# Performance work log

Hardware: AMD Instinct MI355X
Metric: run time of the kernel (lower is better)

The kernel has to match this reference:

```python
import jax, jax.numpy as jnp
import numpy as np

N_HEAD = 16
LN_EPS = 1e-5


def _ln(x, w, b):
    # torch LayerNorm computed in float32 then cast back (see LayerNorm.forward)
    xf = x.astype(jnp.float32)
    mu = jnp.mean(xf, axis=-1, keepdims=True)
    var = jnp.mean(jnp.square(xf - mu), axis=-1, keepdims=True)
    return ((xf - mu) * jax.lax.rsqrt(var + LN_EPS) * w + b).astype(x.dtype)


def setup_inputs() -> dict:
    key = jax.random.key(0)
    ks = jax.random.split(key, 16)
    B, S, C = 4, 1500, 1024
    A = 256  # adapter_dim
    F = 4 * C
    s = 0.02
    return {
        "x": jax.random.normal(ks[0], (B, S, C), jnp.float32),
        "Wq": jax.random.normal(ks[1], (C, C), jnp.float32) * s,
        "bq": jnp.zeros((C,), jnp.float32),
        "Wk": jax.random.normal(ks[2], (C, C), jnp.float32) * s,
        "Wv": jax.random.normal(ks[3], (C, C), jnp.float32) * s,
        "bv": jnp.zeros((C,), jnp.float32),
        "Wo": jax.random.normal(ks[4], (C, C), jnp.float32) * s,
        "bo": jnp.zeros((C,), jnp.float32),
        "ln_attn_w": jnp.ones((C,), jnp.float32),
        "ln_attn_b": jnp.zeros((C,), jnp.float32),
        "W1": jax.random.normal(ks[5], (F, C), jnp.float32) * s,
        "b1": jnp.zeros((F,), jnp.float32),
        "W2": jax.random.normal(ks[6], (C, F), jnp.float32) * s,
        "b2": jnp.zeros((C,), jnp.float32),
        "ln_mlp_w": jnp.ones((C,), jnp.float32),
        "ln_mlp_b": jnp.zeros((C,), jnp.float32),
        "Wds": jax.random.normal(ks[7], (A, C), jnp.float32) * s,
        "bds": jnp.zeros((A,), jnp.float32),
        "Wus": jax.random.normal(ks[8], (C, A), jnp.float32) * s,
        "bus": jnp.zeros((C,), jnp.float32),
    }


def reference(x, Wq, bq, Wk, Wv, bv, Wo, bo, ln_attn_w, ln_attn_b,
              W1, b1, W2, b2, ln_mlp_w, ln_mlp_b, Wds, bds, Wus, bus):
    B, S, C = x.shape
    H = N_HEAD
    D = C // H
    scale = D ** -0.25  # applied to both q and k, per qkv_attention

    # --- self-attention ---
    h = _ln(x, ln_attn_w, ln_attn_b)
    q = (h @ Wq.T + bq).reshape(B, S, H, D) * scale
    k = (h @ Wk.T).reshape(B, S, H, D) * scale  # key has no bias
    v = (h @ Wv.T + bv).reshape(B, S, H, D)
    qk = jnp.einsum("bqhd,bkhd->bhqk", q, k).astype(jnp.float32)
    w = jax.nn.softmax(qk, axis=-1).astype(x.dtype)
    wv = jnp.einsum("bhqk,bkhd->bqhd", w, v).reshape(B, S, C)
    x = x + (wv @ Wo.T + bo)

    # --- MLP (exact GELU, as nn.GELU default) ---
    h = _ln(x, ln_mlp_w, ln_mlp_b)
    x = x + (jax.nn.gelu(h @ W1.T + b1, approximate=False) @ W2.T + b2)

    # --- bottleneck adapter: x + us(gelu(ds(x))) ---
    x = x + (jax.nn.gelu(x @ Wds.T + bds, approximate=False) @ Wus.T + bus)
    return x
```

## Files before the change

kernel.cpp:

```cpp
#include <hip/hip_runtime.h>
#include <hip/hip_bf16.h>
#include <math.h>

typedef __bf16 bf16;
typedef __bf16 bf16x8 __attribute__((ext_vector_type(8)));
typedef float  f32x4  __attribute__((ext_vector_type(4)));

__device__ __forceinline__ bf16x8 zero8() { bf16x8 z = {}; return z; }

__device__ __forceinline__ void load16_lds(const bf16* g, bf16* l) {
    __builtin_amdgcn_global_load_lds(
        (__attribute__((address_space(1))) void*)(g),
        (__attribute__((address_space(3))) void*)(l), 16, 0, 0);
}

__device__ __forceinline__ float gelu_f(float x) {
    float u = 1.5957691216057308f * (x + 0.044715f * x * x * x);
    float e = __expf(u);
    float th = 1.0f - 2.0f / (1.0f + e);
    return 0.5f * x * (1.0f + th);
}

struct ConvArgs {
    const float* src[19];
    bf16* dst[19];
    int n[19];
    int bstart[20];
};
__global__ __launch_bounds__(256) void convert_many(ConvArgs a) {
    int blk = blockIdx.x;
    int s = 0;
    while (blk >= a.bstart[s + 1]) s++;
    const float* src = a.src[s];
    bf16* dst = a.dst[s];
    int n = a.n[s];
    int i0 = (blk - a.bstart[s]) * 2048;
#pragma unroll
    for (int e = 0; e < 8; e++) {
        int i = i0 + threadIdx.x + e * 256;
        if (i < n) dst[i] = (bf16)src[i];
    }
}

__global__ void zero_kernel(bf16* dst, int n) {
    int i = blockIdx.x * blockDim.x + threadIdx.x;
    if (i < n) dst[i] = (bf16)0.0f;
}

template<class XT>
__global__ __launch_bounds__(256) void ln_kernel(
    const XT* __restrict__ X, const bf16* __restrict__ w,
    const bf16* __restrict__ b, bf16* __restrict__ out)
{
    const int C = 1024;
    const int row = blockIdx.x;
    const int tid = threadIdx.x;
    const XT* xr = X + (size_t)row * C;
    float x0 = (float)xr[tid * 4 + 0], x1 = (float)xr[tid * 4 + 1];
    float x2 = (float)xr[tid * 4 + 2], x3 = (float)xr[tid * 4 + 3];
    float s  = x0 + x1 + x2 + x3;
    float sq = x0*x0 + x1*x1 + x2*x2 + x3*x3;
#pragma unroll
    for (int off = 32; off >= 1; off >>= 1) {
        s  += __shfl_xor(s,  off, 64);
        sq += __shfl_xor(sq, off, 64);
    }
    __shared__ float red[8];
    int wave = tid >> 6;
    if ((tid & 63) == 0) { red[wave] = s; red[4 + wave] = sq; }
    __syncthreads();
    float ts = red[0] + red[1] + red[2] + red[3];
    float tq = red[4] + red[5] + red[6] + red[7];
    float mean = ts * (1.0f / C);
    float var  = tq * (1.0f / C) - mean * mean;
    float rstd = rsqrtf(var + 1e-5f);
    float w0 = (float)w[tid*4+0], w1 = (float)w[tid*4+1], w2 = (float)w[tid*4+2], w3 = (float)w[tid*4+3];
    float b0 = (float)b[tid*4+0], b1 = (float)b[tid*4+1], b2 = (float)b[tid*4+2], b3 = (float)b[tid*4+3];
    bf16* orow = out + (size_t)row * C + tid * 4;
    orow[0] = (bf16)((x0 - mean) * rstd * w0 + b0);
    orow[1] = (bf16)((x1 - mean) * rstd * w1 + b1);
    orow[2] = (bf16)((x2 - mean) * rstd * w2 + b2);
    orow[3] = (bf16)((x3 - mean) * rstd * w3 + b3);
}

template<int ACT, int OMODE, class RT, class OT>
__global__ __launch_bounds__(256) void gemm_kernel(
    const bf16* __restrict__ A, const bf16* __restrict__ W,
    const bf16* __restrict__ bias, const RT* __restrict__ resid,
    OT* __restrict__ out, bf16* __restrict__ out_k, bf16* __restrict__ out_v,
    int M, int N, int K, float scale, int gmT, int gnT, int mQ)
{
    const int lin = blockIdx.x;
    const int xcd = lin & 7;
    const int t_  = lin >> 3;
    const int mt_ = (xcd & 3) + 4 * (t_ % mQ);
    const int nt_ = (xcd >> 2) + 2 * (t_ / mQ);
    if (mt_ >= gmT || nt_ >= gnT) return;
    const int m0 = mt_ * 128;
    const int n0 = nt_ * 128;

    __shared__ __align__(16) bf16 As[16 * 512];
    __shared__ __align__(16) bf16 Bs[16 * 512];
    const int tid = threadIdx.x;
    const int wave = tid >> 6, lane = tid & 63;
    const int lane15 = lane & 15, quad = lane >> 4;
    const int wm0 = (wave >> 1) * 64;
    const int wn0 = (wave & 1) * 64;
    f32x4 acc[4][4] = {};

    int ra0 = m0 + (2 * wave)     * 16 + lane15; if (ra0 > M - 1) ra0 = M - 1;
    int ra1 = m0 + (2 * wave + 1) * 16 + lane15; if (ra1 > M - 1) ra1 = M - 1;
    const int rb0 = n0 + (2 * wave)     * 16 + lane15;
    const int rb1 = n0 + (2 * wave + 1) * 16 + lane15;
    const bf16* a0 = A + (size_t)ra0 * K + quad * 8;
    const bf16* a1 = A + (size_t)ra1 * K + quad * 8;
    const bf16* w0 = W + (size_t)rb0 * K + quad * 8;
    const bf16* w1 = W + (size_t)rb1 * K + quad * 8;

    for (int k0 = 0; k0 < K; k0 += 64) {
#pragma unroll
        for (int kk = 0; kk < 2; kk++) {
            load16_lds(a0 + k0 + kk * 32, &As[((2 * wave)     * 2 + kk) * 512]);
            load16_lds(a1 + k0 + kk * 32, &As[((2 * wave + 1) * 2 + kk) * 512]);
            load16_lds(w0 + k0 + kk * 32, &Bs[((2 * wave)     * 2 + kk) * 512]);
            load16_lds(w1 + k0 + kk * 32, &Bs[((2 * wave + 1) * 2 + kk) * 512]);
        }
        __syncthreads();
#pragma unroll
        for (int kk = 0; kk < 2; kk++) {
            bf16x8 af[4], bfr[4];
#pragma unroll
            for (int t = 0; t < 4; t++) {
                af[t]  = *(const bf16x8*)(&As[(((wm0 >> 4) + t) * 2 + kk) * 512 + lane * 8]);
                bfr[t] = *(const bf16x8*)(&Bs[(((wn0 >> 4) + t) * 2 + kk) * 512 + lane * 8]);
            }
#pragma unroll
            for (int mt = 0; mt < 4; mt++)
#pragma unroll
                for (int nt = 0; nt < 4; nt++)
                    acc[mt][nt] = __builtin_amdgcn_mfma_f32_16x16x32_bf16(
                        af[mt], bfr[nt], acc[mt][nt], 0, 0, 0);
        }
        __syncthreads();
    }

#pragma unroll
    for (int mt = 0; mt < 4; mt++) {
#pragma unroll
        for (int r = 0; r < 4; r++) {
            int gm = m0 + wm0 + mt * 16 + quad * 4 + r;
            if (gm >= M) continue;
#pragma unroll
            for (int nt = 0; nt < 4; nt++) {
                int gn = n0 + wn0 + nt * 16 + lane15;
                float v = acc[mt][nt][r];
                if (bias) v += (float)bias[gn];
                if (OMODE == 2) {
                    if (gn < 2048) {
                        v *= scale;
                        if (gn < 1024) v *= 1.4426950408889634f;
                    }
                } else v *= scale;
                if (ACT == 1) v = gelu_f(v);
                if (OMODE == 2) {
                    if (gn < 1024) {
                        ((bf16*)out)[(size_t)gm * 1024 + gn] = (bf16)v;
                    } else if (gn < 2048) {
                        out_k[(size_t)gm * 1024 + (gn - 1024)] = (bf16)v;
                    } else {
                        int gg = gn - 2048;
                        int bb = gm / 1500;
                        int ss = gm - bb * 1500;
                        int hh = gg >> 6, dd = gg & 63;
                        out_v[(((size_t)bb * 16 + hh) * 64 + dd) * 1536 + ss] = (bf16)v;
                    }
                } else {
                    if (resid) v += (float)resid[(size_t)gm * N + gn];
                    out[(size_t)gm * N + gn] = (OT)v;
                }
            }
        }
    }
}

__global__ __launch_bounds__(256) void flash_attn_kernel(
    const bf16* __restrict__ Q, const bf16* __restrict__ Km,
    const bf16* __restrict__ Vt, bf16* __restrict__ O)
{
    const int S = 1500, C = 1024, SP = 1536;
    const int LDP = 72;
    __shared__ __align__(16) bf16 Ks[8 * 512];
    __shared__ __align__(16) bf16 Vs[8 * 512];
    __shared__ __align__(16) bf16 Ps[4 * 16 * LDP];
    const int tid = threadIdx.x;
    const int wave = tid >> 6, lane = tid & 63;
    const int lane15 = lane & 15, quad = lane >> 4;
    const int bh = blockIdx.y;
    const int q0 = blockIdx.x * 64;
    const size_t headoff = (size_t)(bh >> 4) * S * C + (size_t)(bh & 15) * 64;
    const size_t vtoff   = (size_t)bh * 64 * SP;

    bf16x8 qf[2];
    int qr = q0 + wave * 16 + lane15; if (qr > S - 1) qr = S - 1;
    qf[0] = *(const bf16x8*)(Q + headoff + (size_t)qr * C + quad * 8);
    qf[1] = *(const bf16x8*)(Q + headoff + (size_t)qr * C + 32 + quad * 8);

    const bf16* vbase = Vt + vtoff + (size_t)(wave * 16 + lane15) * SP + quad * 8;

    float m_run[4], l_part[4];
    f32x4 o_acc[4] = {};
#pragma unroll
    for (int r = 0; r < 4; r++) { m_run[r] = 4.0f; l_part[r] = 0.0f; }

    for (int kt = 0; kt < 24; kt++) {
        const int j0 = kt * 64;
        int kr = j0 + wave * 16 + lane15; if (kr > S - 1) kr = S - 1;
        const bf16* kbase = Km + headoff + (size_t)kr * C + quad * 8;
#pragma unroll
        for (int kk = 0; kk < 2; kk++) {
            load16_lds(kbase + kk * 32,      &Ks[(wave * 2 + kk) * 512]);
            load16_lds(vbase + j0 + kk * 32, &Vs[(wave * 2 + kk) * 512]);
        }
        __syncthreads();

        f32x4 s[4] = {};
#pragma unroll
        for (int kk = 0; kk < 2; kk++) {
#pragma unroll
            for (int nt = 0; nt < 4; nt++) {
                bf16x8 kf = *(const bf16x8*)(&Ks[(nt * 2 + kk) * 512 + lane * 8]);
                s[nt] = __builtin_amdgcn_mfma_f32_16x16x32_bf16(qf[kk], kf, s[nt], 0, 0, 0);
            }
        }
        if (kt == 23) {
#pragma unroll
            for (int nt = 0; nt < 4; nt++) {
                if (j0 + nt * 16 + lane15 >= S) {
#pragma unroll
                    for (int r = 0; r < 4; r++) s[nt][r] = -1e30f;
                }
            }
        }

        float tm[4];
#pragma unroll
        for (int r = 0; r < 4; r++)
            tm[r] = fmaxf(fmaxf(s[0][r], s[1][r]), fmaxf(s[2][r], s[3][r]));
        bool rec = (tm[0] > m_run[0]) | (tm[1] > m_run[1]) |
                   (tm[2] > m_run[2]) | (tm[3] > m_run[3]);
        if (__any(rec)) {
#pragma unroll
            for (int r = 0; r < 4; r++) {
                float rm = tm[r];
#pragma unroll
                for (int off = 1; off < 16; off <<= 1) rm = fmaxf(rm, __shfl_xor(rm, off, 64));
                float mnew  = fmaxf(m_run[r], rm);
                float alpha = __builtin_amdgcn_exp2f(m_run[r] - mnew);
                m_run[r] = mnew;
                l_part[r] *= alpha;
#pragma unroll
                for (int dt = 0; dt < 4; dt++) o_acc[dt][r] *= alpha;
            }
        }

#pragma unroll
        for (int nt = 0; nt < 4; nt++) {
#pragma unroll
            for (int r = 0; r < 4; r++) {
                float p = __builtin_amdgcn_exp2f(s[nt][r] - m_run[r]);
                l_part[r] += p;
                Ps[wave * 16 * LDP + (quad * 4 + r) * LDP + nt * 16 + lane15] = (bf16)p;
            }
        }
        asm volatile("s_waitcnt lgkmcnt(0)" ::: "memory");
        __builtin_amdgcn_sched_barrier(0);
#pragma unroll
        for (int kk = 0; kk < 2; kk++) {
            bf16x8 pf = *(const bf16x8*)(&Ps[wave * 16 * LDP + lane15 * LDP + kk * 32 + quad * 8]);
#pragma unroll
            for (int dt = 0; dt < 4; dt++) {
                bf16x8 vf = *(const bf16x8*)(&Vs[(dt * 2 + kk) * 512 + lane * 8]);
                o_acc[dt] = __builtin_amdgcn_mfma_f32_16x16x32_bf16(pf, vf, o_acc[dt], 0, 0, 0);
            }
        }
        __syncthreads();
    }

    float l_inv[4];
#pragma unroll
    for (int r = 0; r < 4; r++) {
        float ls = l_part[r];
#pragma unroll
        for (int off = 1; off < 16; off <<= 1) ls += __shfl_xor(ls, off, 64);
        l_inv[r] = 1.0f / ls;
    }

#pragma unroll
    for (int dt = 0; dt < 4; dt++) {
#pragma unroll
        for (int r = 0; r < 4; r++) {
            int row = q0 + wave * 16 + quad * 4 + r;
            if (row < S) {
                float v = o_acc[dt][r] * l_inv[r];
                O[headoff + (size_t)row * C + dt * 16 + lane15] = (bf16)v;
            }
        }
    }
}

extern "C" void kernel_launch(void* const* d_in, const int* in_sizes, int n_in,
                              void* d_out, int out_size, void* d_ws, size_t ws_size,
                              hipStream_t stream) {
    float* out = (float*)d_out;
    const float* x_f32 = (const float*)d_in[0];
    const int M = 6000, Cc = 1024, F = 4096, Aa = 256;
    const size_t MC = (size_t)M * Cc;
    const size_t VT_ELEMS = (size_t)64 * 64 * 1536;
    bf16* ws = (bf16*)d_ws;

    bf16* h1   = ws;
    bf16* kbuf = ws + MC;
    bf16* Vt   = ws + 2 * MC;
    bf16* g    = ws + 2 * MC + VT_ELEMS;
    bf16* q    = (bf16*)d_out;
    bf16* wv   = h1;
    bf16* x1   = q;
    bf16* h2   = kbuf;
    bf16* x2   = Vt;
    bf16* aact = kbuf;

    size_t off = 2 * MC + VT_ELEMS + (size_t)M * F;
    bf16* Wqkv = ws + off; off += (size_t)3 * 1024 * 1024;
    bf16* bqkv = ws + off; off += 3072;
    bf16* sWo  = ws + off; off += (size_t)1024 * 1024;
    bf16* sbo  = ws + off; off += 1024;
    bf16* slnw = ws + off; off += 1024;
    bf16* slnb = ws + off; off += 1024;
    bf16* sW1  = ws + off; off += (size_t)4096 * 1024;
    bf16* sb1  = ws + off; off += 4096;
    bf16* sW2  = ws + off; off += (size_t)1024 * 4096;
    bf16* sb2  = ws + off; off += 1024;
    bf16* sln2w = ws + off; off += 1024;
    bf16* sln2b = ws + off; off += 1024;
    bf16* sWds = ws + off; off += (size_t)256 * 1024;
    bf16* sbds = ws + off; off += 256;
    bf16* sWus = ws + off; off += (size_t)1024 * 256;
    bf16* sbus = ws + off; off += 1024;

    ConvArgs ca;
    const int srcidx[19] = {1, 3, 4, 2, 5, 6, 7, 8, 9, 10, 11, 12, 13, 14, 15, 16, 17, 18, 19};
    bf16* dsts[19] = {Wqkv, Wqkv + 1048576, Wqkv + 2097152, bqkv, bqkv + 2048,
                      sWo, sbo, slnw, slnb, sW1, sb1, sW2, sb2, sln2w, sln2b,
                      sWds, sbds, sWus, sbus};
    int bacc = 0;
    for (int i = 0; i < 19; i++) {
        ca.src[i] = (const float*)d_in[srcidx[i]];
        ca.dst[i] = dsts[i];
        ca.n[i] = in_sizes[srcidx[i]];
        ca.bstart[i] = bacc;
        bacc += (ca.n[i] + 2047) / 2048;
    }
    ca.bstart[19] = bacc;

    dim3 blk(256);
    convert_many<<<bacc, blk, 0, stream>>>(ca);
    zero_kernel<<<4, blk, 0, stream>>>(bqkv + 1024, 1024);

    const float scale = 0.35355339059327373f;
    const int gmT = 47, mQ = 12;
    auto grid_for = [&](int gnT) { int nQ = (gnT + 1) >> 1; return dim3(8 * mQ * nQ); };

    ln_kernel<float><<<M, blk, 0, stream>>>(x_f32, slnw, slnb, h1);
    gemm_kernel<0, 2, bf16, bf16><<<grid_for(24), blk, 0, stream>>>(
        h1, Wqkv, bqkv, (const bf16*)nullptr, q, kbuf, Vt, M, 3072, Cc, scale, gmT, 24, mQ);
    dim3 ga(24, 64);
    flash_attn_kernel<<<ga, blk, 0, stream>>>(q, kbuf, Vt, wv);
    gemm_kernel<0, 0, float, bf16><<<grid_for(8), blk, 0, stream>>>(
        wv, sWo, sbo, x_f32, x1, nullptr, nullptr, M, Cc, Cc, 1.0f, gmT, 8, mQ);
    ln_kernel<bf16><<<M, blk, 0, stream>>>(x1, sln2w, sln2b, h2);
    gemm_kernel<1, 0, bf16, bf16><<<grid_for(32), blk, 0, stream>>>(
        h2, sW1, sb1, (const bf16*)nullptr, g, nullptr, nullptr, M, F, Cc, 1.0f, gmT, 32, mQ);
    gemm_kernel<0, 0, bf16, bf16><<<grid_for(8), blk, 0, stream>>>(
        g, sW2, sb2, x1, x2, nullptr, nullptr, M, Cc, F, 1.0f, gmT, 8, mQ);
    gemm_kernel<1, 0, bf16, bf16><<<grid_for(2), blk, 0, stream>>>(
        x2, sWds, sbds, (const bf16*)nullptr, aact, nullptr, nullptr, M, Aa, Cc, 1.0f, gmT, 2, mQ);
    gemm_kernel<0, 0, bf16, float><<<grid_for(8), blk, 0, stream>>>(
        aact, sWus, sbus, x2, out, nullptr, nullptr, M, Cc, Aa, 1.0f, gmT, 8, mQ);
}
```

Measured before the change: 809.2 us.

## Double-buffer LDS tiles in GEMM and flash attention to overlap loads with MFMA

Both the GEMM and flash-attention kernels now keep two LDS buffers. The next K-tile (or K/V tile) is issued through global_load_lds before the MFMA work on the current tile, so global latency overlaps compute, and each loop step ends with a single wait plus barrier instead of two __syncthreads. This doubles LDS use per block: 64 KB for the GEMM, which may reduce occupancy. The hand-placed vmcnt waits and sched barriers also limit how the compiler can reorder instructions.

```diff
diff --git a/kernel.cpp b/kernel.cpp
--- a/kernel.cpp
+++ b/kernel.cpp
@@ -5,8 +5,6 @@
 typedef __bf16 bf16;
 typedef __bf16 bf16x8 __attribute__((ext_vector_type(8)));
 typedef float  f32x4  __attribute__((ext_vector_type(4)));
-
-__device__ __forceinline__ bf16x8 zero8() { bf16x8 z = {}; return z; }
 
 __device__ __forceinline__ void load16_lds(const bf16* g, bf16* l) {
     __builtin_amdgcn_global_load_lds(
@@ -99,8 +97,8 @@
     const int m0 = mt_ * 128;
     const int n0 = nt_ * 128;
 
-    __shared__ __align__(16) bf16 As[16 * 512];
-    __shared__ __align__(16) bf16 Bs[16 * 512];
+    __shared__ __align__(16) bf16 As[2][16 * 512];
+    __shared__ __align__(16) bf16 Bs[2][16 * 512];
     const int tid = threadIdx.x;
     const int wave = tid >> 6, lane = tid & 63;
     const int lane15 = lane & 15, quad = lane >> 4;
@@ -117,22 +115,32 @@
     const bf16* w0 = W + (size_t)rb0 * K + quad * 8;
     const bf16* w1 = W + (size_t)rb1 * K + quad * 8;
 
-    for (int k0 = 0; k0 < K; k0 += 64) {
+    auto stage = [&](int buf, int k0) {
 #pragma unroll
         for (int kk = 0; kk < 2; kk++) {
-            load16_lds(a0 + k0 + kk * 32, &As[((2 * wave)     * 2 + kk) * 512]);
-            load16_lds(a1 + k0 + kk * 32, &As[((2 * wave + 1) * 2 + kk) * 512]);
-            load16_lds(w0 + k0 + kk * 32, &Bs[((2 * wave)     * 2 + kk) * 512]);
-            load16_lds(w1 + k0 + kk * 32, &Bs[((2 * wave + 1) * 2 + kk) * 512]);
-        }
-        __syncthreads();
+            load16_lds(a0 + k0 + kk * 32, &As[buf][((2 * wave)     * 2 + kk) * 512]);
+            load16_lds(a1 + k0 + kk * 32, &As[buf][((2 * wave + 1) * 2 + kk) * 512]);
+            load16_lds(w0 + k0 + kk * 32, &Bs[buf][((2 * wave)     * 2 + kk) * 512]);
+            load16_lds(w1 + k0 + kk * 32, &Bs[buf][((2 * wave + 1) * 2 + kk) * 512]);
+        }
+    };
+
+    stage(0, 0);
+    asm volatile("s_waitcnt vmcnt(0)" ::: "memory");
+    __builtin_amdgcn_s_barrier();
+    __builtin_amdgcn_sched_barrier(0);
+
+    const int nsteps = K >> 6;
+    int cur = 0;
+    for (int t = 0; t < nsteps; t++) {
+        if (t + 1 < nsteps) stage(cur ^ 1, (t + 1) << 6);
 #pragma unroll
         for (int kk = 0; kk < 2; kk++) {
             bf16x8 af[4], bfr[4];
 #pragma unroll
-            for (int t = 0; t < 4; t++) {
-                af[t]  = *(const bf16x8*)(&As[(((wm0 >> 4) + t) * 2 + kk) * 512 + lane * 8]);
-                bfr[t] = *(const bf16x8*)(&Bs[(((wn0 >> 4) + t) * 2 + kk) * 512 + lane * 8]);
+            for (int tt = 0; tt < 4; tt++) {
+                af[tt]  = *(const bf16x8*)(&As[cur][(((wm0 >> 4) + tt) * 2 + kk) * 512 + lane * 8]);
+                bfr[tt] = *(const bf16x8*)(&Bs[cur][(((wn0 >> 4) + tt) * 2 + kk) * 512 + lane * 8]);
             }
 #pragma unroll
             for (int mt = 0; mt < 4; mt++)
@@ -141,7 +149,12 @@
                     acc[mt][nt] = __builtin_amdgcn_mfma_f32_16x16x32_bf16(
                         af[mt], bfr[nt], acc[mt][nt], 0, 0, 0);
         }
-        __syncthreads();
+        if (t + 1 < nsteps) {
+            asm volatile("s_waitcnt vmcnt(0)" ::: "memory");
+            __builtin_amdgcn_s_barrier();
+            __builtin_amdgcn_sched_barrier(0);
+        }
+        cur ^= 1;
     }
 
 #pragma unroll
@@ -189,8 +202,8 @@
 {
     const int S = 1500, C = 1024, SP = 1536;
     const int LDP = 72;
-    __shared__ __align__(16) bf16 Ks[8 * 512];
-    __shared__ __align__(16) bf16 Vs[8 * 512];
+    __shared__ __align__(16) bf16 Ks[2][8 * 512];
+    __shared__ __align__(16) bf16 Vs[2][8 * 512];
     __shared__ __align__(16) bf16 Ps[4 * 16 * LDP];
     const int tid = threadIdx.x;
     const int wave = tid >> 6, lane = tid & 63;
@@ -207,28 +220,38 @@
 
     const bf16* vbase = Vt + vtoff + (size_t)(wave * 16 + lane15) * SP + quad * 8;
 
-    float m_run[4], l_part[4];
-    f32x4 o_acc[4] = {};
-#pragma unroll
-    for (int r = 0; r < 4; r++) { m_run[r] = 4.0f; l_part[r] = 0.0f; }
-
-    for (int kt = 0; kt < 24; kt++) {
+    auto stageKV = [&](int buf, int kt) {
         const int j0 = kt * 64;
         int kr = j0 + wave * 16 + lane15; if (kr > S - 1) kr = S - 1;
         const bf16* kbase = Km + headoff + (size_t)kr * C + quad * 8;
 #pragma unroll
         for (int kk = 0; kk < 2; kk++) {
-            load16_lds(kbase + kk * 32,      &Ks[(wave * 2 + kk) * 512]);
-            load16_lds(vbase + j0 + kk * 32, &Vs[(wave * 2 + kk) * 512]);
-        }
-        __syncthreads();
+            load16_lds(kbase + kk * 32,      &Ks[buf][(wave * 2 + kk) * 512]);
+            load16_lds(vbase + j0 + kk * 32, &Vs[buf][(wave * 2 + kk) * 512]);
+        }
+    };
+
+    float m_run[4], l_part[4];
+    f32x4 o_acc[4] = {};
+#pragma unroll
+    for (int r = 0; r < 4; r++) { m_run[r] = 4.0f; l_part[r] = 0.0f; }
+
+    stageKV(0, 0);
+    asm volatile("s_waitcnt vmcnt(0)" ::: "memory");
+    __builtin_amdgcn_s_barrier();
+    __builtin_amdgcn_sched_barrier(0);
+
+    int cur = 0;
+    for (int kt = 0; kt < 24; kt++) {
+        if (kt + 1 < 24) stageKV(cur ^ 1, kt + 1);
+        const int j0 = kt * 64;
 
         f32x4 s[4] = {};
 #pragma unroll
         for (int kk = 0; kk < 2; kk++) {
 #pragma unroll
             for (int nt = 0; nt < 4; nt++) {
-                bf16x8 kf = *(const bf16x8*)(&Ks[(nt * 2 + kk) * 512 + lane * 8]);
+                bf16x8 kf = *(const bf16x8*)(&Ks[cur][(nt * 2 + kk) * 512 + lane * 8]);
                 s[nt] = __builtin_amdgcn_mfma_f32_16x16x32_bf16(qf[kk], kf, s[nt], 0, 0, 0);
             }
         }
@@ -279,11 +302,16 @@
             bf16x8 pf = *(const bf16x8*)(&Ps[wave * 16 * LDP + lane15 * LDP + kk * 32 + quad * 8]);
 #pragma unroll
             for (int dt = 0; dt < 4; dt++) {
-                bf16x8 vf = *(const bf16x8*)(&Vs[(dt * 2 + kk) * 512 + lane * 8]);
+                bf16x8 vf = *(const bf16x8*)(&Vs[cur][(dt * 2 + kk) * 512 + lane * 8]);
                 o_acc[dt] = __builtin_amdgcn_mfma_f32_16x16x32_bf16(pf, vf, o_acc[dt], 0, 0, 0);
             }
         }
-        __syncthreads();
+        if (kt + 1 < 24) {
+            asm volatile("s_waitcnt vmcnt(0)" ::: "memory");
+            __builtin_amdgcn_s_barrier();
+            __builtin_amdgcn_sched_barrier(0);
+        }
+        cur ^= 1;
     }
 
     float l_inv[4];
```

Result: no change. 806.1 us (-0.4%).
